# Kernel tuning notes

Measured on AMD Instinct MI355X. Metric: run time of the kernel, lower is better.

Reference implementation:

```python
import jax, jax.numpy as jnp
import numpy as np

N_NODES = 100000
N_EDGES = 6400000
HID = 32


def setup_inputs() -> dict:
    key = jax.random.key(0)
    ks = jax.random.split(key, 24)
    inp = {
        "x_G": jax.random.normal(ks[0], (N_NODES, 1), dtype=jnp.float32),
        "edge_index_G": jax.random.randint(ks[1], (2, N_EDGES), 0, N_NODES, dtype=jnp.int32),
        "x_H": jax.random.normal(ks[2], (N_NODES, 1), dtype=jnp.float32),
        "edge_index_H": jax.random.randint(ks[3], (2, N_EDGES), 0, N_NODES, dtype=jnp.int32),
    }
    ki = 4
    for i in range(3):
        d_in = 1 if i == 0 else HID
        inp[f"W1_{i}"] = jax.random.normal(ks[ki], (d_in, HID), dtype=jnp.float32) / np.sqrt(d_in); ki += 1
        inp[f"b1_{i}"] = jnp.zeros((HID,), dtype=jnp.float32)
        inp[f"W2_{i}"] = jax.random.normal(ks[ki], (HID, HID), dtype=jnp.float32) / np.sqrt(HID); ki += 1
        inp[f"b2_{i}"] = jnp.zeros((HID,), dtype=jnp.float32)
    inp["Wc1"] = jax.random.normal(ks[ki], (2 * HID, HID), dtype=jnp.float32) / np.sqrt(2 * HID); ki += 1
    inp["bc1"] = jnp.zeros((HID,), dtype=jnp.float32)
    inp["Wc2"] = jax.random.normal(ks[ki], (HID, 1), dtype=jnp.float32) / np.sqrt(HID); ki += 1
    inp["bc2"] = jnp.zeros((1,), dtype=jnp.float32)
    return inp


def _encode(x, edge_index, layers):
    n = x.shape[0]
    src, dst = edge_index[0], edge_index[1]
    for (W1, b1, W2, b2) in layers:
        # GIN aggregation: sum of neighbor messages scattered to targets; eps = 0
        agg = jax.ops.segment_sum(x[src], dst, num_segments=n)  # [N, d]
        h = x + agg  # (1 + eps) * x + agg with eps = 0
        h = jax.nn.relu(h @ W1 + b1) @ W2 + b2  # GIN MLP
        x = jax.nn.relu(h)  # outer F.relu in encode loop
    return jnp.sum(x, axis=0, keepdims=True)  # global_add_pool, single graph -> [1, HID]


def reference(x_G, edge_index_G, x_H, edge_index_H,
              W1_0, b1_0, W2_0, b2_0,
              W1_1, b1_1, W2_1, b2_1,
              W1_2, b1_2, W2_2, b2_2,
              Wc1, bc1, Wc2, bc2):
    layers = [(W1_0, b1_0, W2_0, b2_0),
              (W1_1, b1_1, W2_1, b2_1),
              (W1_2, b1_2, W2_2, b2_2)]
    h_G = _encode(x_G, edge_index_G, layers)
    h_H = _encode(x_H, edge_index_H, layers)
    combined = jnp.concatenate([h_G, h_H], axis=1)  # [1, 2*HID]
    out = jax.nn.relu(combined @ Wc1 + bc1) @ Wc2 + bc2
    return jax.nn.sigmoid(out)
```

## Files before the change

### kernel.cpp

```cpp
#include <hip/hip_runtime.h>
#include <hip/hip_bf16.h>
#include <math.h>
#include <string.h>

#define HID 32
#define PSHIFT 8
#define NPB (1 << PSHIFT)
#define MAXP 512
#define SLOTS 17408
#define SBITS 3
#define SBINS (1 << SBITS)
#define NBINS (NPB * SBINS)
#define GS 32
#define HS_ROWS 32
#define COLBUF 3072
#define COLBUF0 6144
typedef unsigned short u16;
typedef unsigned char u8;

__device__ inline float e42f(unsigned b) {
    unsigned u = (b & 0x7fu) << 20;
    float f; memcpy(&f, &u, 4);
    return f * 0x1p120f;
}
__device__ inline unsigned f2e4(float f) {
    f = fminf(f, 448.f);
    float y = f * 0x1p-120f;
    unsigned r; memcpy(&r, &y, 4);
    r = r + 0x7FFFFu + ((r >> 20) & 1u);
    return (r >> 20) & 0x7fu;
}
__device__ inline void acc_e4(float* a, unsigned w) {
    a[0] += e42f(w);
    a[1] += e42f(w >> 8);
    a[2] += e42f(w >> 16);
    a[3] += e42f(w >> 24);
}
__device__ inline u16 f2bf(float f) {
    unsigned x; memcpy(&x, &f, 4);
    unsigned r = x + 0x7fffu + ((x >> 16) & 1u);
    return (u16)(r >> 16);
}

__global__ void zero_kernel(float* __restrict__ p, int n) {
    int i = blockIdx.x * blockDim.x + threadIdx.x;
    if (i < n) p[i] = 0.f;
}
__global__ void init_gcur(int* __restrict__ gcur, int P) {
    int b = blockIdx.x * blockDim.x + threadIdx.x;
    if (b < P) gcur[b * GS] = b * SLOTS;
}

__global__ void partition_edges(const int* __restrict__ src, const int* __restrict__ dst,
                                int* __restrict__ gcur, unsigned* __restrict__ staged,
                                int E, int P) {
    __shared__ int h[4][MAXP];
    __shared__ int hbase[MAXP];
    __shared__ int cur[MAXP];
    __shared__ int gbase[MAXP];
    __shared__ unsigned sortedv[4096];
    __shared__ u16 bktid[4096];
    __shared__ int wsums[4];
    __shared__ int sTotal;
    int t = threadIdx.x, wid = t >> 6, lane = t & 63;
    for (int i = t; i < 4 * MAXP; i += 256) (&h[0][0])[i] = 0;
    __syncthreads();

    int base = blockIdx.x * 4096;
    int4 S[4], D[4];
#pragma unroll
    for (int r = 0; r < 4; r++) {
        int e = base + r * 1024 + t * 4;
        if (e + 3 < E) {
            S[r] = *(const int4*)(src + e);
            D[r] = *(const int4*)(dst + e);
        } else {
            int s0[4], d0[4];
            for (int j = 0; j < 4; j++) {
                int ee = e + j;
                s0[j] = (ee < E) ? src[ee] : -1;
                d0[j] = (ee < E) ? dst[ee] : -1;
            }
            S[r] = make_int4(s0[0], s0[1], s0[2], s0[3]);
            D[r] = make_int4(d0[0], d0[1], d0[2], d0[3]);
        }
        if (D[r].x >= 0) atomicAdd(&h[wid][D[r].x >> PSHIFT], 1);
        if (D[r].y >= 0) atomicAdd(&h[wid][D[r].y >> PSHIFT], 1);
        if (D[r].z >= 0) atomicAdd(&h[wid][D[r].z >> PSHIFT], 1);
        if (D[r].w >= 0) atomicAdd(&h[wid][D[r].w >> PSHIFT], 1);
    }
    __syncthreads();

    int b0 = 2 * t, b1 = 2 * t + 1;
    int t0 = (b0 < P) ? (h[0][b0] + h[1][b0] + h[2][b0] + h[3][b0]) : 0;
    int t1 = (b1 < P) ? (h[0][b1] + h[1][b1] + h[2][b1] + h[3][b1]) : 0;
    int s = t0 + t1;
    int incl = s;
#pragma unroll
    for (int off = 1; off < 64; off <<= 1) {
        int u = __shfl_up(incl, off, 64);
        if (lane >= off) incl += u;
    }
    if (lane == 63) wsums[wid] = incl;
    __syncthreads();
    int woff = 0;
#pragma unroll
    for (int w = 0; w < 4; w++) if (w < wid) woff += wsums[w];
    int excl = woff + incl - s;
    if (b0 < P) { hbase[b0] = excl;      cur[b0] = excl; }
    if (b1 < P) { hbase[b1] = excl + t0; cur[b1] = excl + t0; }
    if (b0 < P && t0) gbase[b0] = atomicAdd(&gcur[b0 * GS], t0);
    if (b1 < P && t1) gbase[b1] = atomicAdd(&gcur[b1 * GS], t1);
    if (t == 255) sTotal = excl + s;
    __syncthreads();

#pragma unroll
    for (int r = 0; r < 4; r++) {
        int ss[4] = { S[r].x, S[r].y, S[r].z, S[r].w };
        int dd[4] = { D[r].x, D[r].y, D[r].z, D[r].w };
#pragma unroll
        for (int j = 0; j < 4; j++) {
            int d = dd[j];
            if (d >= 0) {
                int bk = d >> PSHIFT;
                int pos = atomicAdd(&cur[bk], 1);
                sortedv[pos] = ((unsigned)(d & (NPB - 1)) << 17) | (unsigned)ss[j];
                bktid[pos]   = (u16)bk;
            }
        }
    }
    __syncthreads();

    int total = sTotal;
    for (int i = t; i < total; i += 256) {
        int bk = bktid[i];
        int addr = gbase[bk] + (i - hbase[bk]);
        if (addr < (bk + 1) * SLOTS)
            staged[addr] = sortedv[i];
    }
}

__global__ void scan_buckets(const int* __restrict__ gcur, int* __restrict__ colbase,
                             int* __restrict__ rowptr, int P, int N) {
    __shared__ int wsums[4];
    int t = threadIdx.x, wid = t >> 6, lane = t & 63;
    int b0 = 2 * t, b1 = 2 * t + 1;
    int c0 = 0, c1 = 0;
    if (b0 < P) { c0 = gcur[b0 * GS] - b0 * SLOTS; if (c0 > SLOTS) c0 = SLOTS; }
    if (b1 < P) { c1 = gcur[b1 * GS] - b1 * SLOTS; if (c1 > SLOTS) c1 = SLOTS; }
    int s = c0 + c1;
    int incl = s;
#pragma unroll
    for (int off = 1; off < 64; off <<= 1) {
        int u = __shfl_up(incl, off, 64);
        if (lane >= off) incl += u;
    }
    if (lane == 63) wsums[wid] = incl;
    __syncthreads();
    int woff = 0;
#pragma unroll
    for (int w = 0; w < 4; w++) if (w < wid) woff += wsums[w];
    int excl = woff + incl - s;
    if (b0 < P) colbase[b0] = excl;
    if (b1 < P) colbase[b1] = excl + c0;
    if (t == 255) {
        colbase[P] = excl + s;
        rowptr[N]  = excl + s;
    }
}

__global__ void sort_bucket(const unsigned* __restrict__ staged, const int* __restrict__ gcur,
                            const int* __restrict__ colbase,
                            int* __restrict__ rowptr, int* __restrict__ col, int N) {
    __shared__ int cnt[NBINS];
    __shared__ int wsum[4];
    __shared__ int sorted[SLOTS];
    int b = blockIdx.x;
    int t = threadIdx.x;
    int lane = t & 63, wid = t >> 6;
    int sBeg = b * SLOTS;
    int sEnd = gcur[b * GS]; if (sEnd > sBeg + SLOTS) sEnd = sBeg + SLOTS;
    int total = sEnd - sBeg;
    int colStart = colbase[b];
    int nodeBase = b << PSHIFT;

    for (int i = t; i < NBINS; i += 256) cnt[i] = 0;
    __syncthreads();
    for (int i = sBeg + t; i < sEnd; i += 256) {
        unsigned w = staged[i];
        int key = (int)((w >> 17) << SBITS) | (int)((w & 0x1FFFFu) >> 14);
        atomicAdd(&cnt[key], 1);
    }
    __syncthreads();

    int loc[SBINS]; int tot = 0;
#pragma unroll
    for (int k = 0; k < SBINS; k++) { loc[k] = tot; tot += cnt[(t << SBITS) + k]; }
    int incl = tot;
#pragma unroll
    for (int off = 1; off < 64; off <<= 1) {
        int u = __shfl_up(incl, off, 64);
        if (lane >= off) incl += u;
    }
    if (lane == 63) wsum[wid] = incl;
    __syncthreads();
    int woff = 0;
#pragma unroll
    for (int w = 0; w < 4; w++) if (w < wid) woff += wsum[w];
    int excl = woff + incl - tot;
    int node = nodeBase + t;
    if (node < N) rowptr[node] = colStart + excl;
#pragma unroll
    for (int k = 0; k < SBINS; k++) cnt[(t << SBITS) + k] = excl + loc[k];
    __syncthreads();

    for (int i = sBeg + t; i < sEnd; i += 256) {
        unsigned w = staged[i];
        int key = (int)((w >> 17) << SBITS) | (int)((w & 0x1FFFFu) >> 14);
        int pos = atomicAdd(&cnt[key], 1);
        sorted[pos] = (int)(w & 0x1FFFFu);
    }
    __syncthreads();
    for (int i = t; i < total; i += 256)
        col[colStart + i] = sorted[i];
}

__global__ void mlp0_fused(const int* __restrict__ rowptr, const int* __restrict__ col,
                           const float* __restrict__ x0,
                           const float* __restrict__ W1, const float* __restrict__ b1,
                           const float* __restrict__ W2, const float* __restrict__ b2,
                           u8* __restrict__ out, int n) {
    __shared__ float sW1[HID], sb1[HID], sW2[HID * HID], sb2[HID];
    __shared__ int colbuf[COLBUF0];
    int t = threadIdx.x;
    if (t < HID) { sW1[t] = W1[t]; sb1[t] = b1[t]; sb2[t] = b2[t]; }
    for (int i = t; i < HID * HID; i += blockDim.x) sW2[i] = W2[i];

    int firstNode = blockIdx.x * 64;
    int lastNode  = firstNode + 64; if (lastNode > n) lastNode = n;
    int blockStart = (firstNode < n) ? rowptr[firstNode] : 0;
    int blockEnd   = (firstNode < n) ? rowptr[lastNode] : 0;
    int stagedCnt = blockEnd - blockStart; if (stagedCnt > COLBUF0) stagedCnt = COLBUF0;
    for (int i = t; i < stagedCnt; i += 256) colbuf[i] = col[blockStart + i];
    __syncthreads();

    int node = firstNode + (t >> 2);
    int q    = t & 3;
    int lane = t & 63;
    int base = lane & ~3;
    bool active = node < n;

    float s = 0.f;
    if (active) {
        int beg = rowptr[node], end = rowptr[node + 1];
        int jSplit = blockStart + stagedCnt; if (jSplit > end) jSplit = end;
        int j = beg + q;
        for (; j + 12 < jSplit; j += 16) {
            int c0 = colbuf[j - blockStart];
            int c1 = colbuf[j + 4 - blockStart];
            int c2 = colbuf[j + 8 - blockStart];
            int c3 = colbuf[j + 12 - blockStart];
            s += x0[c0]; s += x0[c1]; s += x0[c2]; s += x0[c3];
        }
        for (; j < jSplit; j += 4) s += x0[colbuf[j - blockStart]];
        for (; j < end; j += 4) s += x0[col[j]];
    }
    s += __shfl_xor(s, 1, 64);
    s += __shfl_xor(s, 2, 64);
    float v = active ? (x0[node] + s) : 0.f;

    float h[8];
#pragma unroll
    for (int i = 0; i < 8; i++) h[i] = fmaxf(fmaf(v, sW1[q * 8 + i], sb1[q * 8 + i]), 0.f);
    float o[8];
#pragma unroll
    for (int i = 0; i < 8; i++) o[i] = sb2[q * 8 + i];
#pragma unroll
    for (int k = 0; k < HID; k++) {
        float hk = __shfl(h[k & 7], base | (k >> 3), 64);
#pragma unroll
        for (int i = 0; i < 8; i++) o[i] = fmaf(hk, sW2[k * HID + q * 8 + i], o[i]);
    }
    if (active) {
        unsigned w0 = f2e4(fmaxf(o[0], 0.f)) | (f2e4(fmaxf(o[1], 0.f)) << 8)
                    | (f2e4(fmaxf(o[2], 0.f)) << 16) | (f2e4(fmaxf(o[3], 0.f)) << 24);
        unsigned w1 = f2e4(fmaxf(o[4], 0.f)) | (f2e4(fmaxf(o[5], 0.f)) << 8)
                    | (f2e4(fmaxf(o[6], 0.f)) << 16) | (f2e4(fmaxf(o[7], 0.f)) << 24);
        uint2 pk = make_uint2(w0, w1);
        *(uint2*)(out + ((size_t)node << 5) + (q << 3)) = pk;
    }
}

template <bool REDUCE>
__global__ void mlp_fused(const int* __restrict__ rowptr, const int* __restrict__ col,
                          const u8* __restrict__ xin,
                          const float* __restrict__ W1, const float* __restrict__ b1,
                          const float* __restrict__ W2, const float* __restrict__ b2,
                          u8* __restrict__ xout, float* __restrict__ hsum, int n) {
    __shared__ float sW1[HID * HID], sb1[HID], sW2[HID * HID], sb2[HID];
    __shared__ int colbuf[COLBUF];
    __shared__ float red[4][HID];
    int t = threadIdx.x;
    for (int i = t; i < HID * HID; i += blockDim.x) { sW1[i] = W1[i]; sW2[i] = W2[i]; }
    if (t < HID) { sb1[t] = b1[t]; sb2[t] = b2[t]; }

    int firstNode = blockIdx.x * 32;
    int lastNode  = firstNode + 32; if (lastNode > n) lastNode = n;
    int blockStart = (firstNode < n) ? rowptr[firstNode] : 0;
    int blockEnd   = (firstNode < n) ? rowptr[lastNode] : 0;
    int stagedCnt = blockEnd - blockStart; if (stagedCnt > COLBUF) stagedCnt = COLBUF;
    for (int i = t; i < stagedCnt; i += 256) colbuf[i] = col[blockStart + i];
    __syncthreads();

    int node = firstNode + (t >> 3);
    int q    = t & 7;
    int lane = t & 63;
    int base = lane & ~7;
    bool active = node < n;

    float va[4];
#pragma unroll
    for (int i = 0; i < 4; i++) va[i] = 0.f;
    if (active) {
        int beg = rowptr[node], end = rowptr[node + 1];
        const u8* xq = xin + (q << 2);
        float a0[4], a1[4], a2[4], a3[4];
#pragma unroll
        for (int i = 0; i < 4; i++) a0[i] = a1[i] = a2[i] = a3[i] = 0.f;
        {
            unsigned w = *(const unsigned*)(xq + ((size_t)node << 5));
            acc_e4(a0, w);
        }
        int jSplit = blockStart + stagedCnt; if (jSplit > end) jSplit = end;
        int j = beg;
        for (; j + 8 <= jSplit; j += 8) {
            int lj = j - blockStart;
            int c0 = colbuf[lj+0], c1 = colbuf[lj+1], c2 = colbuf[lj+2], c3 = colbuf[lj+3];
            int c4 = colbuf[lj+4], c5 = colbuf[lj+5], c6 = colbuf[lj+6], c7 = colbuf[lj+7];
            unsigned w0 = *(const unsigned*)(xq + ((size_t)c0 << 5));
            unsigned w1 = *(const unsigned*)(xq + ((size_t)c1 << 5));
            unsigned w2 = *(const unsigned*)(xq + ((size_t)c2 << 5));
            unsigned w3 = *(const unsigned*)(xq + ((size_t)c3 << 5));
            unsigned w4 = *(const unsigned*)(xq + ((size_t)c4 << 5));
            unsigned w5 = *(const unsigned*)(xq + ((size_t)c5 << 5));
            unsigned w6 = *(const unsigned*)(xq + ((size_t)c6 << 5));
            unsigned w7 = *(const unsigned*)(xq + ((size_t)c7 << 5));
            acc_e4(a0, w0); acc_e4(a1, w1); acc_e4(a2, w2); acc_e4(a3, w3);
            acc_e4(a0, w4); acc_e4(a1, w5); acc_e4(a2, w6); acc_e4(a3, w7);
        }
        for (; j < jSplit; j++) {
            unsigned w = *(const unsigned*)(xq + ((size_t)colbuf[j - blockStart] << 5));
            acc_e4(a0, w);
        }
        for (; j < end; j++) {
            unsigned w = *(const unsigned*)(xq + ((size_t)col[j] << 5));
            acc_e4(a0, w);
        }
#pragma unroll
        for (int i = 0; i < 4; i++) va[i] = (a0[i] + a1[i]) + (a2[i] + a3[i]);
    }

    float h[4];
#pragma unroll
    for (int i = 0; i < 4; i++) h[i] = sb1[q * 4 + i];
#pragma unroll
    for (int k = 0; k < HID; k++) {
        float vk = __shfl(va[k & 3], base | (k >> 2), 64);
#pragma unroll
        for (int i = 0; i < 4; i++) h[i] = fmaf(vk, sW1[k * HID + q * 4 + i], h[i]);
    }
#pragma unroll
    for (int i = 0; i < 4; i++) h[i] = fmaxf(h[i], 0.f);

    float o[4];
#pragma unroll
    for (int i = 0; i < 4; i++) o[i] = sb2[q * 4 + i];
#pragma unroll
    for (int k = 0; k < HID; k++) {
        float hk = __shfl(h[k & 3], base | (k >> 2), 64);
#pragma unroll
        for (int i = 0; i < 4; i++) o[i] = fmaf(hk, sW2[k * HID + q * 4 + i], o[i]);
    }
#pragma unroll
    for (int i = 0; i < 4; i++) o[i] = fmaxf(o[i], 0.f);

    if (REDUCE) {
        if (!active) {
#pragma unroll
            for (int i = 0; i < 4; i++) o[i] = 0.f;
        }
#pragma unroll
        for (int i = 0; i < 4; i++) {
            float v = o[i];
            v += __shfl_xor(v, 8, 64);
            v += __shfl_xor(v, 16, 64);
            v += __shfl_xor(v, 32, 64);
            o[i] = v;
        }
        int wid = t >> 6;
        if (lane < 8) {
#pragma unroll
            for (int i = 0; i < 4; i++) red[wid][lane * 4 + i] = o[i];
        }
        __syncthreads();
        if (t < HID) {
            float s = red[0][t] + red[1][t] + red[2][t] + red[3][t];
            atomicAdd(&hsum[(blockIdx.x & (HS_ROWS - 1)) * (2 * HID) + t], s);
        }
    } else if (active) {
        unsigned pw = f2e4(o[0]) | (f2e4(o[1]) << 8) | (f2e4(o[2]) << 16) | (f2e4(o[3]) << 24);
        *(unsigned*)(xout + ((size_t)node << 5) + (q << 2)) = pw;
    }
}

__global__ void head_kernel(const float* __restrict__ hsumP,
                            const float* __restrict__ Wc1, const float* __restrict__ bc1,
                            const float* __restrict__ Wc2, const float* __restrict__ bc2,
                            float* __restrict__ out) {
    __shared__ float hs[2 * HID];
    int t = threadIdx.x;
    if (t < 2 * HID) {
        float s = 0.f;
        for (int r = 0; r < HS_ROWS; r++) s += hsumP[r * (2 * HID) + t];
        hs[t] = s;
    }
    __syncthreads();
    float val = 0.f;
    if (t < HID) {
        float acc = bc1[t];
        for (int i = 0; i < 2 * HID; i++) acc = fmaf(hs[i], Wc1[i * HID + t], acc);
        val = fmaxf(acc, 0.f) * Wc2[t];
    }
    for (int off = 32; off >= 1; off >>= 1) val += __shfl_xor(val, off, 64);
    if (t == 0) out[0] = 1.f / (1.f + expf(-(val + bc2[0])));
}

extern "C" void kernel_launch(void* const* d_in, const int* in_sizes, int n_in,
                              void* d_out, int out_size, void* d_ws, size_t ws_size,
                              hipStream_t stream) {
    const float* xg[2] = { (const float*)d_in[0], (const float*)d_in[2] };
    const int*   eg[2] = { (const int*)d_in[1],   (const int*)d_in[3] };
    const float* W1[3] = { (const float*)d_in[4], (const float*)d_in[8],  (const float*)d_in[12] };
    const float* b1[3] = { (const float*)d_in[5], (const float*)d_in[9],  (const float*)d_in[13] };
    const float* W2[3] = { (const float*)d_in[6], (const float*)d_in[10], (const float*)d_in[14] };
    const float* b2[3] = { (const float*)d_in[7], (const float*)d_in[11], (const float*)d_in[15] };
    const float* Wc1 = (const float*)d_in[16];
    const float* bc1 = (const float*)d_in[17];
    const float* Wc2 = (const float*)d_in[18];
    const float* bc2 = (const float*)d_in[19];

    const int N = in_sizes[0];
    const int E = in_sizes[1] / 2;
    const int P = (N + NPB - 1) >> PSHIFT;

    u8*       B0      = (u8*)d_ws;
    u8*       B1      = B0 + (size_t)N * 32;
    float*    hsumP   = (float*)(B1 + (size_t)N * 32);
    int*      rowptr  = (int*)(hsumP + HS_ROWS * 2 * HID);
    int*      col     = rowptr + (N + 1);
    int*      colbase = col + (size_t)E;
    int*      gcur    = colbase + (P + 1);
    unsigned* staged  = (unsigned*)(gcur + (size_t)P * GS);

    const int TB = 256;
    dim3 blk(TB);
    int gE4k = (E + 4095) / 4096;
    int gN64 = (N + 63) / 64;
    int gN8  = (N + 31) / 32;
    int gP   = (P + TB - 1) / TB;

    zero_kernel<<<(HS_ROWS * 2 * HID + 255) / 256, 256, 0, stream>>>(hsumP, HS_ROWS * 2 * HID);

    for (int g = 0; g < 2; g++) {
        const float* x0  = xg[g];
        const int*   src = eg[g];
        const int*   dst = src + E;

        init_gcur<<<gP, blk, 0, stream>>>(gcur, P);
        partition_edges<<<gE4k, blk, 0, stream>>>(src, dst, gcur, staged, E, P);
        scan_buckets<<<1, blk, 0, stream>>>(gcur, colbase, rowptr, P, N);
        sort_bucket<<<P, blk, 0, stream>>>(staged, gcur, colbase, rowptr, col, N);

        mlp0_fused<<<gN64, blk, 0, stream>>>(rowptr, col, x0, W1[0], b1[0], W2[0], b2[0], B0, N);

        mlp_fused<false><<<gN8, blk, 0, stream>>>(rowptr, col, B0, W1[1], b1[1], W2[1], b2[1],
                                                  B1, nullptr, N);

        mlp_fused<true><<<gN8, blk, 0, stream>>>(rowptr, col, B1, W1[2], b1[2], W2[2], b2[2],
                                                 nullptr, hsumP + g * HID, N);
    }

    head_kernel<<<1, 64, 0, stream>>>(hsumP, Wc1, bc1, Wc2, bc2, (float*)d_out);
}
```

Baseline: 578.6 us.

## Process 16K edges per partition block with one global atomic reservation per bucket

Each partition block now handles four 4096-edge chunks. It first histograms all 16K destinations, reserves global bucket space once per bucket with a single atomicAdd, then sorts and scatters each chunk in turn while advancing a running per-bucket offset. This cuts global atomics on gcur by about four times and makes the runs written per bucket into staged longer, which should give better-coalesced writes. In exchange, dst is read twice, there are more block-level barriers, and the grid is four times smaller, which may reduce occupancy and latency hiding.

```diff
diff --git a/kernel.cpp b/kernel.cpp
--- a/kernel.cpp
+++ b/kernel.cpp
@@ -15,6 +15,7 @@
 #define HS_ROWS 32
 #define COLBUF 3072
 #define COLBUF0 6144
+#define EPB 16384
 typedef unsigned short u16;
 typedef unsigned char u8;
 
@@ -36,11 +37,6 @@
     a[2] += e42f(w >> 16);
     a[3] += e42f(w >> 24);
 }
-__device__ inline u16 f2bf(float f) {
-    unsigned x; memcpy(&x, &f, 4);
-    unsigned r = x + 0x7fffu + ((x >> 16) & 1u);
-    return (u16)(r >> 16);
-}
 
 __global__ void zero_kernel(float* __restrict__ p, int n) {
     int i = blockIdx.x * blockDim.x + threadIdx.x;
@@ -54,89 +50,114 @@
 __global__ void partition_edges(const int* __restrict__ src, const int* __restrict__ dst,
                                 int* __restrict__ gcur, unsigned* __restrict__ staged,
                                 int E, int P) {
-    __shared__ int h[4][MAXP];
+    __shared__ int hc[4][MAXP];
     __shared__ int hbase[MAXP];
     __shared__ int cur[MAXP];
-    __shared__ int gbase[MAXP];
+    __shared__ int run[MAXP];
     __shared__ unsigned sortedv[4096];
     __shared__ u16 bktid[4096];
     __shared__ int wsums[4];
     __shared__ int sTotal;
     int t = threadIdx.x, wid = t >> 6, lane = t & 63;
-    for (int i = t; i < 4 * MAXP; i += 256) (&h[0][0])[i] = 0;
-    __syncthreads();
-
-    int base = blockIdx.x * 4096;
-    int4 S[4], D[4];
-#pragma unroll
-    for (int r = 0; r < 4; r++) {
-        int e = base + r * 1024 + t * 4;
-        if (e + 3 < E) {
-            S[r] = *(const int4*)(src + e);
-            D[r] = *(const int4*)(dst + e);
-        } else {
-            int s0[4], d0[4];
+    for (int i = t; i < 4 * MAXP; i += 256) (&hc[0][0])[i] = 0;
+    __syncthreads();
+
+    int base = blockIdx.x * EPB;
+
+    {
+        int cbase = base + wid * 4096;
+#pragma unroll
+        for (int k = 0; k < 16; k++) {
+            int e = cbase + k * 256 + lane * 4;
+            int4 D;
+            if (e + 3 < E) {
+                D = *(const int4*)(dst + e);
+            } else {
+                int d0[4];
+                for (int j = 0; j < 4; j++) d0[j] = (e + j < E) ? dst[e + j] : -1;
+                D = make_int4(d0[0], d0[1], d0[2], d0[3]);
+            }
+            if (D.x >= 0) atomicAdd(&hc[wid][D.x >> PSHIFT], 1);
+            if (D.y >= 0) atomicAdd(&hc[wid][D.y >> PSHIFT], 1);
+            if (D.z >= 0) atomicAdd(&hc[wid][D.z >> PSHIFT], 1);
+            if (D.w >= 0) atomicAdd(&hc[wid][D.w >> PSHIFT], 1);
+        }
+    }
+    __syncthreads();
+
+    int b0 = 2 * t, b1 = 2 * t + 1;
+    int tot0 = 0, tot1 = 0;
+    if (b0 < P) tot0 = hc[0][b0] + hc[1][b0] + hc[2][b0] + hc[3][b0];
+    if (b1 < P) tot1 = hc[0][b1] + hc[1][b1] + hc[2][b1] + hc[3][b1];
+    if (b0 < P && tot0) run[b0] = atomicAdd(&gcur[b0 * GS], tot0);
+    if (b1 < P && tot1) run[b1] = atomicAdd(&gcur[b1 * GS], tot1);
+
+    for (int c = 0; c < 4; c++) {
+        int t0 = (b0 < P) ? hc[c][b0] : 0;
+        int t1 = (b1 < P) ? hc[c][b1] : 0;
+        int s = t0 + t1;
+        int incl = s;
+#pragma unroll
+        for (int off = 1; off < 64; off <<= 1) {
+            int u = __shfl_up(incl, off, 64);
+            if (lane >= off) incl += u;
+        }
+        if (lane == 63) wsums[wid] = incl;
+        __syncthreads();
+        int woff = 0;
+#pragma unroll
+        for (int w = 0; w < 4; w++) if (w < wid) woff += wsums[w];
+        int excl = woff + incl - s;
+        if (b0 < P) { hbase[b0] = excl;      cur[b0] = excl; }
+        if (b1 < P) { hbase[b1] = excl + t0; cur[b1] = excl + t0; }
+        if (t == 255) sTotal = excl + s;
+        __syncthreads();
+
+#pragma unroll
+        for (int r = 0; r < 4; r++) {
+            int e = base + c * 4096 + r * 1024 + t * 4;
+            int4 S4, D4;
+            if (e + 3 < E) {
+                S4 = *(const int4*)(src + e);
+                D4 = *(const int4*)(dst + e);
+            } else {
+                int s0[4], d0[4];
+                for (int j = 0; j < 4; j++) {
+                    int ee = e + j;
+                    s0[j] = (ee < E) ? src[ee] : -1;
+                    d0[j] = (ee < E) ? dst[ee] : -1;
+                }
+                S4 = make_int4(s0[0], s0[1], s0[2], s0[3]);
+                D4 = make_int4(d0[0], d0[1], d0[2], d0[3]);
+            }
+            int ss[4] = { S4.x, S4.y, S4.z, S4.w };
+            int dd[4] = { D4.x, D4.y, D4.z, D4.w };
+#pragma unroll
             for (int j = 0; j < 4; j++) {
-                int ee = e + j;
-                s0[j] = (ee < E) ? src[ee] : -1;
-                d0[j] = (ee < E) ? dst[ee] : -1;
+                int d = dd[j];
+                if (d >= 0) {
+                    int bk = d >> PSHIFT;
+                    int pos = atomicAdd(&cur[bk], 1);
+                    sortedv[pos] = ((unsigned)(d & (NPB - 1)) << 17) | (unsigned)ss[j];
+                    bktid[pos]   = (u16)bk;
+                }
             }
-            S[r] = make_int4(s0[0], s0[1], s0[2], s0[3]);
-            D[r] = make_int4(d0[0], d0[1], d0[2], d0[3]);
-        }
-        if (D[r].x >= 0) atomicAdd(&h[wid][D[r].x >> PSHIFT], 1);
-        if (D[r].y >= 0) atomicAdd(&h[wid][D[r].y >> PSHIFT], 1);
-        if (D[r].z >= 0) atomicAdd(&h[wid][D[r].z >> PSHIFT], 1);
-        if (D[r].w >= 0) atomicAdd(&h[wid][D[r].w >> PSHIFT], 1);
-    }
-    __syncthreads();
-
-    int b0 = 2 * t, b1 = 2 * t + 1;
-    int t0 = (b0 < P) ? (h[0][b0] + h[1][b0] + h[2][b0] + h[3][b0]) : 0;
-    int t1 = (b1 < P) ? (h[0][b1] + h[1][b1] + h[2][b1] + h[3][b1]) : 0;
-    int s = t0 + t1;
-    int incl = s;
-#pragma unroll
-    for (int off = 1; off < 64; off <<= 1) {
-        int u = __shfl_up(incl, off, 64);
-        if (lane >= off) incl += u;
-    }
-    if (lane == 63) wsums[wid] = incl;
-    __syncthreads();
-    int woff = 0;
-#pragma unroll
-    for (int w = 0; w < 4; w++) if (w < wid) woff += wsums[w];
-    int excl = woff + incl - s;
-    if (b0 < P) { hbase[b0] = excl;      cur[b0] = excl; }
-    if (b1 < P) { hbase[b1] = excl + t0; cur[b1] = excl + t0; }
-    if (b0 < P && t0) gbase[b0] = atomicAdd(&gcur[b0 * GS], t0);
-    if (b1 < P && t1) gbase[b1] = atomicAdd(&gcur[b1 * GS], t1);
-    if (t == 255) sTotal = excl + s;
-    __syncthreads();
-
-#pragma unroll
-    for (int r = 0; r < 4; r++) {
-        int ss[4] = { S[r].x, S[r].y, S[r].z, S[r].w };
-        int dd[4] = { D[r].x, D[r].y, D[r].z, D[r].w };
-#pragma unroll
-        for (int j = 0; j < 4; j++) {
-            int d = dd[j];
-            if (d >= 0) {
-                int bk = d >> PSHIFT;
-                int pos = atomicAdd(&cur[bk], 1);
-                sortedv[pos] = ((unsigned)(d & (NPB - 1)) << 17) | (unsigned)ss[j];
-                bktid[pos]   = (u16)bk;
-            }
-        }
-    }
-    __syncthreads();
-
-    int total = sTotal;
-    for (int i = t; i < total; i += 256) {
-        int bk = bktid[i];
-        int addr = gbase[bk] + (i - hbase[bk]);
-        if (addr < (bk + 1) * SLOTS)
-            staged[addr] = sortedv[i];
+        }
+        __syncthreads();
+
+        int total = sTotal;
+        for (int i = t; i < total; i += 256) {
+            int bk = bktid[i];
+            int addr = run[bk] + (i - hbase[bk]);
+            if (addr < (bk + 1) * SLOTS)
+                staged[addr] = sortedv[i];
+        }
+        __syncthreads();
+
+        if (c < 3) {
+            if (b0 < P && t0) run[b0] += t0;
+            if (b1 < P && t1) run[b1] += t1;
+        }
     }
 }
 
@@ -464,7 +485,7 @@
 
     const int TB = 256;
     dim3 blk(TB);
-    int gE4k = (E + 4095) / 4096;
+    int gE16k = (E + EPB - 1) / EPB;
     int gN64 = (N + 63) / 64;
     int gN8  = (N + 31) / 32;
     int gP   = (P + TB - 1) / TB;
@@ -477,7 +498,7 @@
         const int*   dst = src + E;
 
         init_gcur<<<gP, blk, 0, stream>>>(gcur, P);
-        partition_edges<<<gE4k, blk, 0, stream>>>(src, dst, gcur, staged, E, P);
+        partition_edges<<<gE16k, blk, 0, stream>>>(src, dst, gcur, staged, E, P);
         scan_buckets<<<1, blk, 0, stream>>>(gcur, colbase, rowptr, P, N);
         sort_bucket<<<P, blk, 0, stream>>>(staged, gcur, colbase, rowptr, col, N);
 
```

Result: no change. 586.6 us (+1.4%).
